# Optimization experiments

Hardware: AMD Instinct MI355X
Metric: run time of the kernel (lower is better)

Reference implementation:

```python
import jax, jax.numpy as jnp
import numpy as np

H, W = 384, 384          # render resolution (init h, w)
TH, TW = 1024, 1024      # texture resolution
N, V, F = 2, 2048, 2048  # batch, vertices/texcoords, faces
CHUNK = 32               # faces per rasterization scan step
EPS = 1e-8


def setup_inputs() -> dict:
    key = jax.random.key(0)
    k = jax.random.split(key, 5)
    # vertices in front of camera, z ~ 3
    v = jax.random.normal(k[0], (N, V, 3), jnp.float32) * jnp.array([0.5, 0.5, 0.3], jnp.float32) + jnp.array([0.0, 0.0, 3.0], jnp.float32)
    tex = jax.random.uniform(k[1], (N, 3, TH, TW), jnp.float32)
    campos = jnp.zeros((N, 3), jnp.float32)
    camrot = jnp.broadcast_to(jnp.eye(3, dtype=jnp.float32), (N, 3, 3))
    focal = jnp.broadcast_to(400.0 * jnp.eye(2, dtype=jnp.float32), (N, 2, 2))
    princpt = jnp.broadcast_to(jnp.array([W / 2.0, H / 2.0], jnp.float32), (N, 2))
    vt = jax.random.uniform(k[2], (V, 2), jnp.float32)
    vt = vt.at[:, 1].set(1.0 - vt[:, 1])  # flip_uvs=True applied at init
    vi = jax.random.randint(k[3], (F, 3), 0, V, jnp.int32)
    vti = jax.random.randint(k[4], (F, 3), 0, V, jnp.int32)
    return {"v": v, "tex": tex, "campos": campos, "camrot": camrot, "focal": focal, "princpt": princpt, "vt": vt, "vi": vi, "vti": vti}


def _bary(x0, y0, x1, y1, x2, y2, px, py):
    # signed-area-normalized screen-space barycentrics (both windings accepted)
    area = (x1 - x0) * (y2 - y0) - (y1 - y0) * (x2 - x0)
    ok = jnp.abs(area) > 1e-9
    inv = 1.0 / jnp.where(ok, area, 1.0)
    b0 = ((x2 - x1) * (py - y1) - (y2 - y1) * (px - x1)) * inv
    b1 = ((x0 - x2) * (py - y2) - (y0 - y2) * (px - x2)) * inv
    b2 = ((x1 - x0) * (py - y0) - (y1 - y0) * (px - x0)) * inv
    return b0, b1, b2, ok


def _rasterize_one(v_pix, vi):
    # z-buffered rasterization via scan over face chunks; pixel centers at +0.5
    px = jnp.arange(W, dtype=jnp.float32)[None, None, :] + 0.5
    py = jnp.arange(H, dtype=jnp.float32)[None, :, None] + 0.5
    nch = F // CHUNK
    fids = jnp.arange(F, dtype=jnp.int32).reshape(nch, CHUNK)
    vic = vi.reshape(nch, CHUNK, 3)

    def body(carry, inp):
        zbuf, ibuf = carry
        fid, f = inp
        tri = v_pix[f]                       # [CHUNK,3,3]
        x = tri[:, :, 0][:, :, None, None]
        y = tri[:, :, 1][:, :, None, None]
        z = tri[:, :, 2][:, :, None, None]
        b0, b1, b2, ok = _bary(x[:, 0], y[:, 0], x[:, 1], y[:, 1], x[:, 2], y[:, 2], px, py)
        inside = (b0 >= 0) & (b1 >= 0) & (b2 >= 0) & ok
        zinv = b0 / z[:, 0] + b1 / z[:, 1] + b2 / z[:, 2]  # perspective-correct 1/depth
        d = jnp.where(inside & (zinv > EPS), 1.0 / jnp.maximum(zinv, EPS), jnp.inf)
        amin = jnp.argmin(d, axis=0)
        dmin = jnp.min(d, axis=0)
        upd = dmin < zbuf
        return (jnp.where(upd, dmin, zbuf), jnp.where(upd, fid[amin], ibuf)), None

    init = (jnp.full((H, W), jnp.inf, jnp.float32), jnp.full((H, W), -1, jnp.int32))
    (_, ib), _ = jax.lax.scan(body, init, (fids, vic))
    return ib


def _render_one(v_pix, vi, idx):
    # recompute perspective-correct barycentrics / depth for winning faces (differentiable)
    px = jnp.arange(W, dtype=jnp.float32)[None, :] + 0.5
    py = jnp.arange(H, dtype=jnp.float32)[:, None] + 0.5
    tri = v_pix[vi[jnp.maximum(idx, 0)]]     # [H,W,3,3]
    x, y, z = tri[..., 0], tri[..., 1], tri[..., 2]
    b0, b1, b2, ok = _bary(x[..., 0], y[..., 0], x[..., 1], y[..., 1], x[..., 2], y[..., 2], px, py)
    w0, w1, w2 = b0 / z[..., 0], b1 / z[..., 1], b2 / z[..., 2]
    zinv = jnp.maximum(w0 + w1 + w2, EPS)
    mask = idx >= 0
    depth = jnp.where(mask, 1.0 / zinv, 0.0)
    bary = jnp.where(mask[None], jnp.stack([w0, w1, w2], 0) / zinv[None], 0.0)  # [3,H,W]
    return depth, bary


def _interp_one(attr, fvi, idx, bary):
    vals = attr[fvi[jnp.maximum(idx, 0)]]    # [H,W,3,C]
    return jnp.einsum('hwkc,khw->chw', vals, bary)


def _grid_sample_one(tex, grid):
    # bilinear, align_corners=False, padding_mode='border'
    ix = ((grid[..., 0] + 1.0) * TW - 1.0) * 0.5
    iy = ((grid[..., 1] + 1.0) * TH - 1.0) * 0.5
    ix0 = jnp.floor(ix); iy0 = jnp.floor(iy)
    wx = ix - ix0; wy = iy - iy0
    x0 = jnp.clip(ix0.astype(jnp.int32), 0, TW - 1)
    x1 = jnp.clip(ix0.astype(jnp.int32) + 1, 0, TW - 1)
    y0 = jnp.clip(iy0.astype(jnp.int32), 0, TH - 1)
    y1 = jnp.clip(iy0.astype(jnp.int32) + 1, 0, TH - 1)
    g = lambda yi, xi: tex[:, yi, xi]        # [C,H,W]
    return (g(y0, x0) * (1 - wx) * (1 - wy) + g(y0, x1) * wx * (1 - wy)
            + g(y1, x0) * (1 - wx) * wy + g(y1, x1) * wx * wy)


_rasterize = jax.vmap(_rasterize_one, (0, None))
_render = jax.vmap(_render_one, (0, None, 0))
_interp = jax.vmap(_interp_one, (0, None, 0, 0))
_grid_sample = jax.vmap(_grid_sample_one)


def reference(v, tex, campos, camrot, focal, princpt, vt, vi, vti):
    # camera transform: v_cam = R (v - campos); v_pix = focal @ (xy/z) + princpt, z preserved
    v_cam = jnp.einsum('nij,nvj->nvi', camrot, v - campos[:, None, :])
    z = v_cam[..., 2:3]
    xy = jnp.einsum('nij,nvj->nvi', focal, v_cam[..., :2] / z) + princpt[:, None, :]
    v_pix = jnp.concatenate([xy, z], axis=-1)
    idx = _rasterize(jax.lax.stop_gradient(v_pix), vi)   # rasterize under no_grad
    mask = idx >= 0
    depth_img, bary_img = _render(v_pix, vi, idx)
    uv = jnp.broadcast_to(2.0 * vt - 1.0, (v.shape[0], vt.shape[0], 2))
    vt_img = _interp(uv, vti, idx, bary_img).transpose(0, 2, 3, 1)  # NHWC uv grid
    image = _grid_sample(tex, vt_img) * mask[:, None].astype(tex.dtype)
    return image
```

## Files before the change

kernel.cpp:

```cpp
#include <hip/hip_runtime.h>
#include <math.h>

#pragma clang fp contract(off)

#define NN 2
#define VV 2048
#define FF 2048
#define HH 384
#define WW 384
#define TH 1024
#define TW 1024
#define EPSD 1e-08
#define SLICES 16
#define FPS (FF / SLICES)
#define SETUP_BLOCKS ((NN * FF + 255) / 256)
#define CLEAR_BLOCKS ((NN * HH * WW + 255) / 256)

__device__ __forceinline__ float mulr(float a, float b) {
    float p = a * b;
    asm("" : "+v"(p));
    return p;
}


__global__ __launch_bounds__(256) void setup_and_clear(
    const float* __restrict__ v, const float* __restrict__ campos,
    const float* __restrict__ camrot, const float* __restrict__ focal,
    const float* __restrict__ princpt, const int* __restrict__ vi,
    const float* __restrict__ vt, const int* __restrict__ vti,
    double* __restrict__ dface, double* __restrict__ uvface,
    float4* __restrict__ cull, unsigned long long* __restrict__ keybuf)
{
#pragma clang fp contract(off)
    if (blockIdx.x >= SETUP_BLOCKS) {
        int idx = (blockIdx.x - SETUP_BLOCKS) * 256 + threadIdx.x;
        if (idx < NN * HH * WW) keybuf[idx] = 0ull;
        return;
    }
    int t = blockIdx.x * blockDim.x + threadIdx.x;
    if (t >= NN * FF) return;
    int n = t / FF, f = t % FF;
    const float* cr = camrot + n * 9;
    const float* cp = campos + n * 3;
    const float* fo = focal + n * 4;
    const float* pp = princpt + n * 2;
    float X[3], Y[3], Z[3];
    for (int k = 0; k < 3; ++k) {
        int vid = vi[f * 3 + k];
        const float* vp = v + ((size_t)n * VV + vid) * 3;
        float d0 = vp[0] - cp[0];
        float d1 = vp[1] - cp[1];
        float d2 = vp[2] - cp[2];
        float c0 = (mulr(cr[0], d0) + mulr(cr[1], d1)) + mulr(cr[2], d2);
        float c1 = (mulr(cr[3], d0) + mulr(cr[4], d1)) + mulr(cr[5], d2);
        float c2 = (mulr(cr[6], d0) + mulr(cr[7], d1)) + mulr(cr[8], d2);
        float u = c0 / c2;
        float w = c1 / c2;
        X[k] = (mulr(fo[0], u) + mulr(fo[1], w)) + pp[0];
        Y[k] = (mulr(fo[2], u) + mulr(fo[3], w)) + pp[1];
        Z[k] = c2;
    }
    float area = mulr(X[1] - X[0], Y[2] - Y[0]) - mulr(Y[1] - Y[0], X[2] - X[0]);
    bool ok = fabsf(area) > 1e-9f;
    float inv = ok ? (1.0f / area) : __builtin_nanf("");
    float e0x = X[2] - X[1], e0y = Y[2] - Y[1];
    float e1x = X[0] - X[2], e1y = Y[0] - Y[2];
    float e2x = X[1] - X[0], e2y = Y[1] - Y[0];
    double invd = (double)inv;
    double e0xd = (double)e0x, e0yd = (double)e0y;
    double e1xd = (double)e1x, e1yd = (double)e1y;
    double e2xd = (double)e2x, e2yd = (double)e2y;
    double x0d = (double)X[0], y0d = (double)Y[0];
    double x1d = (double)X[1], y1d = (double)Y[1];
    double x2d = (double)X[2], y2d = (double)Y[2];
    double rz0 = 1.0 / (double)Z[0];
    double rz1 = 1.0 / (double)Z[1];
    double rz2 = 1.0 / (double)Z[2];
    double Gx0 = -e0yd * invd, Gy0 = e0xd * invd, Gc0 = (e0yd * x1d - e0xd * y1d) * invd;
    double Gx1 = -e1yd * invd, Gy1 = e1xd * invd, Gc1 = (e1yd * x2d - e1xd * y2d) * invd;
    double Gx2 = -e2yd * invd, Gy2 = e2xd * invd, Gc2 = (e2yd * x0d - e2xd * y0d) * invd;
    double Zx = Gx0 * rz0 + Gx1 * rz1 + Gx2 * rz2;
    double Zy = Gy0 * rz0 + Gy1 * rz1 + Gy2 * rz2;
    double Zc = Gc0 * rz0 + Gc1 * rz1 + Gc2 * rz2;
    double* dd = dface + (size_t)t * 16;
    dd[0] = Gx0; dd[1] = Gy0; dd[2] = Gc0;
    dd[3] = Gx1; dd[4] = Gy1; dd[5] = Gc1;
    dd[6] = Gx2; dd[7] = Gy2; dd[8] = Gc2;
    dd[9] = Zx; dd[10] = Zy; dd[11] = Zc;
    dd[12] = 0.0; dd[13] = 0.0; dd[14] = 0.0; dd[15] = 0.0;
    int i0 = vti[f * 3 + 0], i1 = vti[f * 3 + 1], i2 = vti[f * 3 + 2];
    double u0d = (double)(2.0f * vt[i0 * 2 + 0] - 1.0f), v0d = (double)(2.0f * vt[i0 * 2 + 1] - 1.0f);
    double u1d = (double)(2.0f * vt[i1 * 2 + 0] - 1.0f), v1d = (double)(2.0f * vt[i1 * 2 + 1] - 1.0f);
    double u2d = (double)(2.0f * vt[i2 * 2 + 0] - 1.0f), v2d = (double)(2.0f * vt[i2 * 2 + 1] - 1.0f);
    double W0x = Gx0 * rz0, W0y = Gy0 * rz0, W0c = Gc0 * rz0;
    double W1x = Gx1 * rz1, W1y = Gy1 * rz1, W1c = Gc1 * rz1;
    double W2x = Gx2 * rz2, W2y = Gy2 * rz2, W2c = Gc2 * rz2;
    double* uv = uvface + (size_t)t * 8;
    uv[0] = (u0d * W0x + u1d * W1x) + u2d * W2x;
    uv[1] = (u0d * W0y + u1d * W1y) + u2d * W2y;
    uv[2] = (u0d * W0c + u1d * W1c) + u2d * W2c;
    uv[3] = (v0d * W0x + v1d * W1x) + v2d * W2x;
    uv[4] = (v0d * W0y + v1d * W1y) + v2d * W2y;
    uv[5] = (v0d * W0c + v1d * W1c) + v2d * W2c;
    uv[6] = 0.0; uv[7] = 0.0;
    float s = (area > 0.0f) ? 1.0f : -1.0f;
    float A0 = -e0y * s, B0 = e0x * s;
    float C0 = s * (float)(e0yd * x1d - e0xd * y1d);
    float A1 = -e1y * s, B1 = e1x * s;
    float C1 = s * (float)(e1yd * x2d - e1xd * y2d);
    float A2 = -e2y * s, B2 = e2x * s;
    float C2 = s * (float)(e2yd * x0d - e2xd * y0d);
    if (!ok) { C0 = -3e30f; C1 = -3e30f; C2 = -3e30f; }
    float xmn = fminf(fminf(X[0], X[1]), X[2]);
    float xmx = fmaxf(fmaxf(X[0], X[1]), X[2]);
    float ymn = fminf(fminf(Y[0], Y[1]), Y[2]);
    float ymx = fmaxf(fmaxf(Y[0], Y[1]), Y[2]);
    float4* cu = cull + (size_t)t * 4;
    cu[0] = make_float4(xmn, ymn, xmx, ymx);
    cu[1] = make_float4(A0, B0, C0, A1);
    cu[2] = make_float4(B1, C1, A2, B2);
    cu[3] = make_float4(C2, 0.0f, 0.0f, 0.0f);
}

__device__ __forceinline__ bool edge_keep(float A, float B, float C,
                                          float xlo, float xhi, float ylo, float yhi) {
    float m = A * ((A > 0.0f) ? xhi : xlo) + B * ((B > 0.0f) ? yhi : ylo) + C;
    return m >= -1.0f;
}

__global__ __launch_bounds__(256) void raster(
    const double* __restrict__ dface, const float4* __restrict__ cull,
    unsigned long long* __restrict__ keybuf)
{
#pragma clang fp contract(fast)
    __shared__ int s_cnt[4];
    __shared__ int s_list[4][FPS];
    int nz = blockIdx.z;
    int n = nz / SLICES, slice = nz % SLICES;
    int tx0 = blockIdx.x * 16, ty0 = blockIdx.y * 16;
    int tid = threadIdx.x;
    int lane = tid & 63;
    int wv = tid >> 6;
    if (tid < 4) s_cnt[tid] = 0;
    __syncthreads();
    float xlo = (float)tx0, ylo = (float)ty0;
    {
        int f = slice + (tid & 127) * SLICES;
        int qbase = (tid >> 7) * 2;
        const float4* cu = cull + ((size_t)n * FF + f) * 4;
        float4 bb = cu[0];
        if (bb.x <= xlo + 16.0f && bb.z >= xlo && bb.y <= ylo + 16.0f && bb.w >= ylo) {
            float4 c1 = cu[1], c2 = cu[2], c3 = cu[3];
            #pragma unroll
            for (int qq = 0; qq < 2; ++qq) {
                int q = qbase + qq;
                float qxlo = xlo + (float)((q & 1) * 8), qxhi = qxlo + 8.0f;
                float qylo = ylo + (float)((q >> 1) * 8), qyhi = qylo + 8.0f;
                if (bb.x <= qxhi && bb.z >= qxlo && bb.y <= qyhi && bb.w >= qylo &&
                    edge_keep(c1.x, c1.y, c1.z, qxlo, qxhi, qylo, qyhi) &&
                    edge_keep(c1.w, c2.x, c2.y, qxlo, qxhi, qylo, qyhi) &&
                    edge_keep(c2.z, c2.w, c3.x, qxlo, qxhi, qylo, qyhi)) {
                    int p = atomicAdd(&s_cnt[q], 1);
                    s_list[q][p] = f;
                }
            }
        }
    }
    __syncthreads();
    int cnt = s_cnt[wv];
    int lst0 = s_list[wv][lane];
    int lst1 = s_list[wv][lane + 64];
    int qx0 = tx0 + (wv & 1) * 8;
    int qy0 = ty0 + (wv >> 1) * 8;
    double px = (double)(qx0 + (lane & 7)) + 0.5;
    double py = (double)(qy0 + (lane >> 3)) + 0.5;
    unsigned long long best = 0ull;
    const double* gbase = dface + (size_t)n * FF * 16;
    for (int i = 0; i < cnt; ++i) {
        int src = (i < 64) ? lst0 : lst1;
        int fid = __builtin_amdgcn_readlane(src, i & 63);
        const double* g = gbase + (size_t)fid * 16;
        double zinv = g[9] * px + (g[10] * py + g[11]);
        unsigned long long key =
            ((unsigned long long)__double_as_longlong(zinv) & ~0x7FFull)
            | (unsigned long long)(2047 - fid);
        bool cand = (zinv > EPSD) && (key > best);
        if (__any(cand)) {
            double b0 = g[0] * px + (g[1] * py + g[2]);
            double b1 = g[3] * px + (g[4] * py + g[5]);
            double b2 = g[6] * px + (g[7] * py + g[8]);
            if (cand && fmin(fmin(b0, b1), b2) >= 0.0) best = key;
        }
    }
    if (best) {
        int x = qx0 + (lane & 7), y = qy0 + (lane >> 3);
        atomicMax(keybuf + ((size_t)n * HH + y) * WW + x, best);
    }
}

__global__ __launch_bounds__(256) void render(
    const double* __restrict__ dface, const double* __restrict__ uvface,
    const unsigned long long* __restrict__ keybuf,
    const float* __restrict__ tex, float* __restrict__ out)
{
    int t = blockIdx.x * blockDim.x + threadIdx.x;
    if (t >= NN * HH * WW) return;
    int n = t / (HH * WW);
    int p = t % (HH * WW);
    int y = p / WW, x = p % WW;
    unsigned long long k = keybuf[t];
    int f = k ? (2047 - (int)(k & 0x7FFull)) : -1;
    size_t o0 = ((size_t)(n * 3 + 0) * HH + y) * WW + x;
    size_t o1 = ((size_t)(n * 3 + 1) * HH + y) * WW + x;
    size_t o2 = ((size_t)(n * 3 + 2) * HH + y) * WW + x;
    if (f < 0) {
        out[o0] = 0.0f; out[o1] = 0.0f; out[o2] = 0.0f;
        return;
    }
    const double* g = dface + ((size_t)n * FF + f) * 16;
    const double* uv = uvface + ((size_t)n * FF + f) * 8;
    double px = (double)x + 0.5, py = (double)y + 0.5;
    double s = g[9] * px + (g[10] * py + g[11]);
    double zq = fmax(s, EPSD);
    double rzq = 1.0 / zq;
    double gx = (uv[0] * px + (uv[1] * py + uv[2])) * rzq;
    double gy = (uv[3] * px + (uv[4] * py + uv[5])) * rzq;
    double ix = ((gx + 1.0) * (double)TW - 1.0) * 0.5;
    double iy = ((gy + 1.0) * (double)TH - 1.0) * 0.5;
    double fx0 = floor(ix), fy0 = floor(iy);
    double wx = ix - fx0, wy = iy - fy0;
    int x0 = min(max((int)fx0, 0), TW - 1);
    int x1 = min(max((int)fx0 + 1, 0), TW - 1);
    int y0 = min(max((int)fy0, 0), TH - 1);
    int y1 = min(max((int)fy0 + 1, 0), TH - 1);
    double omwx = 1.0 - wx, omwy = 1.0 - wy;
    bool pair = (x1 == x0 + 1);
    #pragma unroll
    for (int c = 0; c < 3; ++c) {
        const float* tc = tex + ((size_t)n * 3 + c) * TH * TW;
        float g00, g01, g10, g11;
        if (pair) {
            float2 r0 = *(const float2*)(tc + (size_t)y0 * TW + x0);
            float2 r1 = *(const float2*)(tc + (size_t)y1 * TW + x0);
            g00 = r0.x; g01 = r0.y; g10 = r1.x; g11 = r1.y;
        } else {
            g00 = tc[(size_t)y0 * TW + x0];
            g01 = tc[(size_t)y0 * TW + x1];
            g10 = tc[(size_t)y1 * TW + x0];
            g11 = tc[(size_t)y1 * TW + x1];
        }
        double val = ((((double)g00 * omwx) * omwy + ((double)g01 * wx) * omwy)
                      + ((double)g10 * omwx) * wy) + ((double)g11 * wx) * wy;
        size_t oo = (c == 0) ? o0 : ((c == 1) ? o1 : o2);
        out[oo] = (float)val;
    }
}

extern "C" void kernel_launch(void* const* d_in, const int* in_sizes, int n_in,
                              void* d_out, int out_size, void* d_ws, size_t ws_size,
                              hipStream_t stream) {
    const float* v = (const float*)d_in[0];
    const float* tex = (const float*)d_in[1];
    const float* campos = (const float*)d_in[2];
    const float* camrot = (const float*)d_in[3];
    const float* focal = (const float*)d_in[4];
    const float* princpt = (const float*)d_in[5];
    const float* vt = (const float*)d_in[6];
    const int* vi = (const int*)d_in[7];
    const int* vti = (const int*)d_in[8];
    float* out = (float*)d_out;

    char* ws = (char*)d_ws;
    double* dface = (double*)ws;
    double* uvface = (double*)(ws + 524288);
    float4* cull = (float4*)(ws + 524288 + 262144);
    unsigned long long* keybuf =
        (unsigned long long*)(ws + 524288 + 262144 + 262144);

    setup_and_clear<<<dim3(SETUP_BLOCKS + CLEAR_BLOCKS), dim3(256), 0, stream>>>(
        v, campos, camrot, focal, princpt, vi, vt, vti, dface, uvface, cull, keybuf);
    raster<<<dim3(WW / 16, HH / 16, NN * SLICES), dim3(256), 0, stream>>>(
        dface, cull, keybuf);
    render<<<dim3((NN * HH * WW + 255) / 256), dim3(256), 0, stream>>>(
        dface, uvface, keybuf, tex, out);
}
```

Measured before the change: 143.0 us.

## Cull occluded faces per quad using fully-covering triangles' depth bound

During per-tile binning, each face now also checks whether it fully covers an 8x8 quad, via conservative edge tests, and has positive depth there. If so, it records a conservative lower bound on the winning key in shared memory. Faces whose maximum inverse depth over the quad cannot beat that bound are dropped from the quad's list, and the per-pixel search starts from the bound. This shortens the per-pixel face loop but adds a double-precision depth fetch, extra atomics and a barrier in the binning phase, with some risk of subtle correctness issues from the key packing.

```diff
diff --git a/kernel.cpp b/kernel.cpp
--- a/kernel.cpp
+++ b/kernel.cpp
@@ -127,6 +127,11 @@
     float m = A * ((A > 0.0f) ? xhi : xlo) + B * ((B > 0.0f) ? yhi : ylo) + C;
     return m >= -1.0f;
 }
+__device__ __forceinline__ bool edge_cover(float A, float B, float C,
+                                           float xlo, float xhi, float ylo, float yhi) {
+    float m = A * ((A > 0.0f) ? xlo : xhi) + B * ((B > 0.0f) ? ylo : yhi) + C;
+    return m >= 1.0f;
+}
 
 __global__ __launch_bounds__(256) void raster(
     const double* __restrict__ dface, const float4* __restrict__ cull,
@@ -135,36 +140,87 @@
 #pragma clang fp contract(fast)
     __shared__ int s_cnt[4];
     __shared__ int s_list[4][FPS];
+    __shared__ unsigned long long s_B[4];
     int nz = blockIdx.z;
     int n = nz / SLICES, slice = nz % SLICES;
     int tx0 = blockIdx.x * 16, ty0 = blockIdx.y * 16;
     int tid = threadIdx.x;
     int lane = tid & 63;
     int wv = tid >> 6;
-    if (tid < 4) s_cnt[tid] = 0;
+    if (tid < 4) { s_cnt[tid] = 0; s_B[tid] = 0ull; }
     __syncthreads();
     float xlo = (float)tx0, ylo = (float)ty0;
+    int f = slice + (tid & 127) * SLICES;
+    int qbase = (tid >> 7) * 2;
+    bool keep0 = false, keep1 = false;
+    unsigned long long ub0 = 0ull, ub1 = 0ull;
     {
-        int f = slice + (tid & 127) * SLICES;
-        int qbase = (tid >> 7) * 2;
         const float4* cu = cull + ((size_t)n * FF + f) * 4;
         float4 bb = cu[0];
         if (bb.x <= xlo + 16.0f && bb.z >= xlo && bb.y <= ylo + 16.0f && bb.w >= ylo) {
             float4 c1 = cu[1], c2 = cu[2], c3 = cu[3];
-            #pragma unroll
-            for (int qq = 0; qq < 2; ++qq) {
-                int q = qbase + qq;
-                float qxlo = xlo + (float)((q & 1) * 8), qxhi = qxlo + 8.0f;
-                float qylo = ylo + (float)((q >> 1) * 8), qyhi = qylo + 8.0f;
-                if (bb.x <= qxhi && bb.z >= qxlo && bb.y <= qyhi && bb.w >= qylo &&
-                    edge_keep(c1.x, c1.y, c1.z, qxlo, qxhi, qylo, qyhi) &&
-                    edge_keep(c1.w, c2.x, c2.y, qxlo, qxhi, qylo, qyhi) &&
-                    edge_keep(c2.z, c2.w, c3.x, qxlo, qxhi, qylo, qyhi)) {
-                    int p = atomicAdd(&s_cnt[q], 1);
-                    s_list[q][p] = f;
+            float qylo = ylo + (float)((qbase >> 1) * 8), qyhi = qylo + 8.0f;
+            float xl0 = xlo, xh0 = xlo + 8.0f;
+            float xl1 = xh0, xh1 = xlo + 16.0f;
+            bool ov0 = bb.x <= xh0 && bb.z >= xl0 && bb.y <= qyhi && bb.w >= qylo &&
+                       edge_keep(c1.x, c1.y, c1.z, xl0, xh0, qylo, qyhi) &&
+                       edge_keep(c1.w, c2.x, c2.y, xl0, xh0, qylo, qyhi) &&
+                       edge_keep(c2.z, c2.w, c3.x, xl0, xh0, qylo, qyhi);
+            bool ov1 = bb.x <= xh1 && bb.z >= xl1 && bb.y <= qyhi && bb.w >= qylo &&
+                       edge_keep(c1.x, c1.y, c1.z, xl1, xh1, qylo, qyhi) &&
+                       edge_keep(c1.w, c2.x, c2.y, xl1, xh1, qylo, qyhi) &&
+                       edge_keep(c2.z, c2.w, c3.x, xl1, xh1, qylo, qyhi);
+            if (ov0 || ov1) {
+                const double* gz = dface + ((size_t)n * FF + f) * 16;
+                double Zx = gz[9], Zy = gz[10], Zc = gz[11];
+                double qyD = (double)qylo;
+                double z00 = Zx * (double)tx0 + (Zy * qyD + Zc);
+                double dx8 = Zx * 8.0, dy8 = Zy * 8.0;
+                double za0 = z00, za1 = z00 + dx8, za2 = za1 + dx8;
+                double zb0 = za0 + dy8, zb1 = za1 + dy8, zb2 = za2 + dy8;
+                if (ov0) {
+                    double zmn = fmin(fmin(za0, za1), fmin(zb0, zb1));
+                    double zmx = fmax(fmax(za0, za1), fmax(zb0, zb1));
+                    if (zmx > EPSD) {
+                        keep0 = true;
+                        ub0 = ((unsigned long long)__double_as_longlong(zmx) & ~0x7FFull) | 2047ull;
+                        if (zmn > EPSD &&
+                            edge_cover(c1.x, c1.y, c1.z, xl0, xh0, qylo, qyhi) &&
+                            edge_cover(c1.w, c2.x, c2.y, xl0, xh0, qylo, qyhi) &&
+                            edge_cover(c2.z, c2.w, c3.x, xl0, xh0, qylo, qyhi)) {
+                            unsigned long long pz =
+                                ((unsigned long long)__double_as_longlong(zmn) & ~0x7FFull) - 1ull;
+                            atomicMax(&s_B[qbase], pz);
+                        }
+                    }
+                }
+                if (ov1) {
+                    double zmn = fmin(fmin(za1, za2), fmin(zb1, zb2));
+                    double zmx = fmax(fmax(za1, za2), fmax(zb1, zb2));
+                    if (zmx > EPSD) {
+                        keep1 = true;
+                        ub1 = ((unsigned long long)__double_as_longlong(zmx) & ~0x7FFull) | 2047ull;
+                        if (zmn > EPSD &&
+                            edge_cover(c1.x, c1.y, c1.z, xl1, xh1, qylo, qyhi) &&
+                            edge_cover(c1.w, c2.x, c2.y, xl1, xh1, qylo, qyhi) &&
+                            edge_cover(c2.z, c2.w, c3.x, xl1, xh1, qylo, qyhi)) {
+                            unsigned long long pz =
+                                ((unsigned long long)__double_as_longlong(zmn) & ~0x7FFull) - 1ull;
+                            atomicMax(&s_B[qbase + 1], pz);
+                        }
+                    }
                 }
             }
         }
+    }
+    __syncthreads();
+    if (keep0 && ub0 > s_B[qbase]) {
+        int p = atomicAdd(&s_cnt[qbase], 1);
+        s_list[qbase][p] = f;
+    }
+    if (keep1 && ub1 > s_B[qbase + 1]) {
+        int p = atomicAdd(&s_cnt[qbase + 1], 1);
+        s_list[qbase + 1][p] = f;
     }
     __syncthreads();
     int cnt = s_cnt[wv];
@@ -174,7 +230,8 @@
     int qy0 = ty0 + (wv >> 1) * 8;
     double px = (double)(qx0 + (lane & 7)) + 0.5;
     double py = (double)(qy0 + (lane >> 3)) + 0.5;
-    unsigned long long best = 0ull;
+    unsigned long long binit = s_B[wv];
+    unsigned long long best = binit;
     const double* gbase = dface + (size_t)n * FF * 16;
     for (int i = 0; i < cnt; ++i) {
         int src = (i < 64) ? lst0 : lst1;
@@ -192,7 +249,7 @@
             if (cand && fmin(fmin(b0, b1), b2) >= 0.0) best = key;
         }
     }
-    if (best) {
+    if (best > binit) {
         int x = qx0 + (lane & 7), y = qy0 + (lane >> 3);
         atomicMax(keybuf + ((size_t)n * HH + y) * WW + x, best);
     }
```

After: 135.8 us. -5.0%, faster.
